# Performance work log

Hardware: AMD Instinct MI355X
Metric: run time of the kernel (lower is better)

The kernel has to match this reference:

```python
import jax, jax.numpy as jnp
import numpy as np

EPS = 1e-9

def setup_inputs() -> dict:
    key = jax.random.key(0)
    k1, k2, k3, k4 = jax.random.split(key, 4)
    B, D, M, R, C = 1024, 16, 4, 4096, 64
    x = jax.random.normal(k1, (B, D), dtype=jnp.float32)
    centers = jax.random.normal(k2, (D, M), dtype=jnp.float32)
    widths = jnp.ones((D, M), dtype=jnp.float32)
    consequents = jax.random.normal(k3, (R, D + 1, C), dtype=jnp.float32)
    rules = jax.random.randint(k4, (R, D), 0, M)  # rule -> MF index per input dim
    return {"x": x, "centers": centers, "widths": widths,
            "consequents": consequents, "rules": rules}

def reference(x, centers, widths, consequents, rules):
    B, D = x.shape
    # Gaussian membership values: [B, D, M]
    mfs = jnp.exp(-(x[:, :, None] - centers[None]) ** 2 / (2.0 * widths[None] ** 2)) + EPS
    # Gather per-rule MFs: rule_mfs[b, d, r] = mfs[b, d, rules[r, d]] -> [B, D, R]
    rule_mfs = jnp.take_along_axis(mfs, rules.T[None, :, :], axis=2)
    # Product firing strengths and normalization: [B, R]
    fs = jnp.prod(rule_mfs, axis=1)
    nfs = fs / (fs.sum(axis=1, keepdims=True) + EPS)
    # Extended input with bias: [B, D+1]
    x_ext = jnp.concatenate([x, jnp.ones((B, 1), dtype=x.dtype)], axis=1)
    # NOTE: faithful to the original torch code: 'bi,rjc->brc' has no shared
    # contraction index, so it sums x_ext over i and consequents over j.
    rule_out = jnp.einsum('br,brc->bc', nfs,
                          jnp.einsum('bi,rjc->brc', x_ext, consequents))
    return rule_out, nfs, x_ext
```

## Files before the change

### kernel.cpp

```cpp
#include <hip/hip_runtime.h>
#include <hip/hip_bf16.h>

typedef __attribute__((ext_vector_type(8))) short short8;
typedef __attribute__((ext_vector_type(4))) short short4v;
typedef __attribute__((ext_vector_type(4))) float floatx4;
typedef __attribute__((ext_vector_type(4))) unsigned int uintx4;
typedef __attribute__((ext_vector_type(4))) int intx4;
typedef unsigned int u32;
typedef unsigned short u16;

#define NB 1024
#define ND 16
#define NM 4
#define NR 4096
#define NC 64
#define EPSF 1e-9f
#define KS 8

__device__ inline u16 f2bf(float f) {
    u32 u;
    __builtin_memcpy(&u, &f, 4);
    u32 lsb = (u >> 16) & 1;
    u += 0x7fffu + lsb;
    return (u16)(u >> 16);
}

__global__ __launch_bounds__(256) void k_pack(const int* __restrict__ rules,
                                              u32* __restrict__ packed) {
    int r = blockIdx.x * 256 + threadIdx.x;
    const int* q = rules + (size_t)r * ND;
    u32 pk = 0;
#pragma unroll
    for (int i = 0; i < 4; ++i) {
        intx4 v = *(const intx4*)(q + i * 4);
#pragma unroll
        for (int e = 0; e < 4; ++e) pk |= ((u32)(v[e] & 3)) << (2 * (i * 4 + e));
    }
    packed[r] = pk;
}

__global__ __launch_bounds__(256) void k_mid(const float* __restrict__ cons,
                                             const float* __restrict__ x,
                                             const float* __restrict__ centers,
                                             const float* __restrict__ widths,
                                             const u32* __restrict__ packed,
                                             u16* __restrict__ s_consT,
                                             float* __restrict__ out_nfs,
                                             float* __restrict__ out_xe,
                                             float* __restrict__ sx) {
    __shared__ u16 tile[16][68];
    __shared__ float xv[16];
    __shared__ float mftab[64];
    __shared__ float gtab[1024];
    __shared__ float wred[4];
    __shared__ float s_inv;
    int bid = blockIdx.x;
    int tid = threadIdx.x;
    if (bid < 256) {
        int rbase = bid * 16;
        int c = tid & 63;
        int rr = tid >> 6;
#pragma unroll
        for (int it = 0; it < 4; ++it, rr += 4) {
            const float* p = cons + (size_t)(rbase + rr) * (ND + 1) * NC + c;
            float s = 0.f;
#pragma unroll
            for (int j = 0; j < ND + 1; ++j) s += p[j * NC];
            tile[rr][c] = f2bf(s);
        }
        __syncthreads();
        int cc = tid >> 2;
        int r0 = (tid & 3) * 4;
        short4v v;
#pragma unroll
        for (int e = 0; e < 4; ++e) v[e] = (short)tile[r0 + e][cc];
        *(short4v*)(s_consT + (size_t)cc * NR + rbase + r0) = v;
        return;
    }
    int b = bid - 256;
    if (tid < 16) {
        float raw = x[b * 16 + tid];
        xv[tid] = raw;
        out_xe[b * 17 + tid] = raw;
    }
    if (tid == 16) out_xe[b * 17 + 16] = 1.0f;
    __syncthreads();
    if (tid < 64) {
        float diff = xv[tid >> 2] - centers[tid];
        float w = widths[tid];
        mftab[tid] = __expf(-diff * diff / (2.f * w * w)) + EPSF;
    }
    __syncthreads();
    for (int idx = tid; idx < 1024; idx += 256) {
        int g = idx >> 8, i = idx & 255;
        const float* mf = mftab + g * 16;
        gtab[idx] = mf[0 + (i & 3)] * mf[4 + ((i >> 2) & 3)] *
                    mf[8 + ((i >> 4) & 3)] * mf[12 + ((i >> 6) & 3)];
    }
    __syncthreads();
    floatx4 f[4];
    float lsum = 0.f;
#pragma unroll
    for (int it = 0; it < 4; ++it) {
        int r = it * 1024 + tid * 4;
        uintx4 p = *(const uintx4*)(packed + r);
#pragma unroll
        for (int e = 0; e < 4; ++e) {
            u32 pk = p[e];
            f[it][e] = gtab[pk & 255] * gtab[256 + ((pk >> 8) & 255)] *
                       gtab[512 + ((pk >> 16) & 255)] * gtab[768 + (pk >> 24)];
            lsum += f[it][e];
        }
    }
    for (int off = 32; off; off >>= 1) lsum += __shfl_down(lsum, off, 64);
    if ((tid & 63) == 0) wred[tid >> 6] = lsum;
    __syncthreads();
    if (tid == 0) s_inv = 1.f / (wred[0] + wred[1] + wred[2] + wred[3] + EPSF);
    __syncthreads();
    float inv = s_inv;
    if (tid == 0) {
        float s = 1.f;
        for (int i = 0; i < 16; ++i) s += xv[i];
        sx[b] = s;
    }
    float* on = out_nfs + (size_t)b * NR;
#pragma unroll
    for (int it = 0; it < 4; ++it) {
        int r = it * 1024 + tid * 4;
        floatx4 v;
#pragma unroll
        for (int e = 0; e < 4; ++e) v[e] = f[it][e] * inv;
        *(floatx4*)(on + r) = v;
    }
}

__global__ __launch_bounds__(256) void k_gemm(const float* __restrict__ nfs,
                                              const u16* __restrict__ s_consT,
                                              float* __restrict__ part) {
    __shared__ float red[2][16][64];
    int rt = blockIdx.x;
    int ks = blockIdx.y;
    int tid = threadIdx.x;
    int wid = tid >> 6, lane = tid & 63;
    int rsub = wid & 1, khalf = wid >> 1;
    int row = rt * 32 + rsub * 16 + (lane & 15);
    int k0 = ks * 512 + khalf * 256 + (lane >> 4) * 8;
    const float* aptr = nfs + (size_t)row * NR + k0;
    const u16* bptr = s_consT + (size_t)(lane & 15) * NR + k0;

    floatx4 acc[4] = {};
    floatx4 a0 = *(const floatx4*)(aptr);
    floatx4 a1 = *(const floatx4*)(aptr + 4);
    short8 bv[4], bn[4];
#pragma unroll
    for (int cb = 0; cb < 4; ++cb) bv[cb] = *(const short8*)(bptr + (size_t)cb * 16 * NR);
#pragma unroll
    for (int t = 0; t < 8; ++t) {
        floatx4 na0, na1;
        if (t < 7) {
            na0 = *(const floatx4*)(aptr + (t + 1) * 32);
            na1 = *(const floatx4*)(aptr + (t + 1) * 32 + 4);
#pragma unroll
            for (int cb = 0; cb < 4; ++cb)
                bn[cb] = *(const short8*)(bptr + (size_t)cb * 16 * NR + (t + 1) * 32);
        }
        short8 af;
#pragma unroll
        for (int e = 0; e < 4; ++e) {
            af[e] = (short)f2bf(a0[e]);
            af[e + 4] = (short)f2bf(a1[e]);
        }
#pragma unroll
        for (int cb = 0; cb < 4; ++cb)
            acc[cb] = __builtin_amdgcn_mfma_f32_16x16x32_bf16(af, bv[cb], acc[cb], 0, 0, 0);
        if (t < 7) {
            a0 = na0; a1 = na1;
#pragma unroll
            for (int cb = 0; cb < 4; ++cb) bv[cb] = bn[cb];
        }
    }
    int rloc = (lane >> 4) * 4;
    if (khalf == 1) {
#pragma unroll
        for (int cb = 0; cb < 4; ++cb)
#pragma unroll
            for (int reg = 0; reg < 4; ++reg)
                red[rsub][rloc + reg][cb * 16 + (lane & 15)] = acc[cb][reg];
    }
    __syncthreads();
    if (khalf == 0) {
        float* po = part + (size_t)ks * (NB * NC);
#pragma unroll
        for (int cb = 0; cb < 4; ++cb)
#pragma unroll
            for (int reg = 0; reg < 4; ++reg) {
                float v = acc[cb][reg] + red[rsub][rloc + reg][cb * 16 + (lane & 15)];
                po[(size_t)(rt * 32 + rsub * 16 + rloc + reg) * NC + cb * 16 + (lane & 15)] = v;
            }
    }
}

__global__ __launch_bounds__(256) void k_out(const float* __restrict__ part,
                                             const float* __restrict__ sx,
                                             float* __restrict__ out0) {
    int t = blockIdx.x * 256 + threadIdx.x;
    float a = 0.f;
#pragma unroll
    for (int ks = 0; ks < KS; ++ks) a += part[(size_t)ks * (NB * NC) + t];
    out0[t] = a * sx[t >> 6];
}

extern "C" void kernel_launch(void* const* d_in, const int* in_sizes, int n_in,
                              void* d_out, int out_size, void* d_ws, size_t ws_size,
                              hipStream_t stream) {
    const float* x = (const float*)d_in[0];
    const float* centers = (const float*)d_in[1];
    const float* widths = (const float*)d_in[2];
    const float* cons = (const float*)d_in[3];
    const int* rules = (const int*)d_in[4];

    float* out = (float*)d_out;
    float* out_rule = out;
    float* out_nfs = out + NB * NC;
    float* out_xe = out + NB * NC + NB * NR;

    char* ws = (char*)d_ws;
    u16* s_consT = (u16*)ws;
    u32* packed = (u32*)(ws + (512 << 10));
    float* sx = (float*)(ws + (512 << 10) + (16 << 10));
    float* part = (float*)(ws + (512 << 10) + (24 << 10));

    k_pack<<<NR / 256, 256, 0, stream>>>(rules, packed);
    k_mid<<<256 + NB, 256, 0, stream>>>(cons, x, centers, widths, packed,
                                        s_consT, out_nfs, out_xe, sx);
    k_gemm<<<dim3(32, KS), 256, 0, stream>>>(out_nfs, s_consT, part);
    k_out<<<(NB * NC) / 256, 256, 0, stream>>>(part, sx, out_rule);
}
```

Before: 31.94 us.

## Widen blocks to 512 threads and double GEMM split-K to 16 slices

```diff
diff --git a/kernel.cpp b/kernel.cpp
--- a/kernel.cpp
+++ b/kernel.cpp
@@ -15,7 +15,7 @@
 #define NR 4096
 #define NC 64
 #define EPSF 1e-9f
-#define KS 8
+#define KS 16
 
 __device__ inline u16 f2bf(float f) {
     u32 u;
@@ -39,7 +39,7 @@
     packed[r] = pk;
 }
 
-__global__ __launch_bounds__(256) void k_mid(const float* __restrict__ cons,
+__global__ __launch_bounds__(512) void k_mid(const float* __restrict__ cons,
                                              const float* __restrict__ x,
                                              const float* __restrict__ centers,
                                              const float* __restrict__ widths,
@@ -48,20 +48,20 @@
                                              float* __restrict__ out_nfs,
                                              float* __restrict__ out_xe,
                                              float* __restrict__ sx) {
-    __shared__ u16 tile[16][68];
+    __shared__ u16 tile[32][68];
     __shared__ float xv[16];
     __shared__ float mftab[64];
     __shared__ float gtab[1024];
-    __shared__ float wred[4];
+    __shared__ float wred[8];
     __shared__ float s_inv;
     int bid = blockIdx.x;
     int tid = threadIdx.x;
-    if (bid < 256) {
-        int rbase = bid * 16;
+    if (bid < 128) {
+        int rbase = bid * 32;
         int c = tid & 63;
         int rr = tid >> 6;
 #pragma unroll
-        for (int it = 0; it < 4; ++it, rr += 4) {
+        for (int it = 0; it < 4; ++it, rr += 8) {
             const float* p = cons + (size_t)(rbase + rr) * (ND + 1) * NC + c;
             float s = 0.f;
 #pragma unroll
@@ -69,15 +69,15 @@
             tile[rr][c] = f2bf(s);
         }
         __syncthreads();
-        int cc = tid >> 2;
-        int r0 = (tid & 3) * 4;
+        int cc = tid >> 3;
+        int r0 = (tid & 7) * 4;
         short4v v;
 #pragma unroll
         for (int e = 0; e < 4; ++e) v[e] = (short)tile[r0 + e][cc];
         *(short4v*)(s_consT + (size_t)cc * NR + rbase + r0) = v;
         return;
     }
-    int b = bid - 256;
+    int b = bid - 128;
     if (tid < 16) {
         float raw = x[b * 16 + tid];
         xv[tid] = raw;
@@ -91,19 +91,21 @@
         mftab[tid] = __expf(-diff * diff / (2.f * w * w)) + EPSF;
     }
     __syncthreads();
-    for (int idx = tid; idx < 1024; idx += 256) {
+#pragma unroll
+    for (int it = 0; it < 2; ++it) {
+        int idx = it * 512 + tid;
         int g = idx >> 8, i = idx & 255;
         const float* mf = mftab + g * 16;
         gtab[idx] = mf[0 + (i & 3)] * mf[4 + ((i >> 2) & 3)] *
                     mf[8 + ((i >> 4) & 3)] * mf[12 + ((i >> 6) & 3)];
     }
     __syncthreads();
-    floatx4 f[4];
+    int r0 = tid * 8;
+    floatx4 f[2];
     float lsum = 0.f;
 #pragma unroll
-    for (int it = 0; it < 4; ++it) {
-        int r = it * 1024 + tid * 4;
-        uintx4 p = *(const uintx4*)(packed + r);
+    for (int it = 0; it < 2; ++it) {
+        uintx4 p = *(const uintx4*)(packed + r0 + it * 4);
 #pragma unroll
         for (int e = 0; e < 4; ++e) {
             u32 pk = p[e];
@@ -115,87 +117,87 @@
     for (int off = 32; off; off >>= 1) lsum += __shfl_down(lsum, off, 64);
     if ((tid & 63) == 0) wred[tid >> 6] = lsum;
     __syncthreads();
-    if (tid == 0) s_inv = 1.f / (wred[0] + wred[1] + wred[2] + wred[3] + EPSF);
+    if (tid == 0) {
+        float t = 0.f;
+#pragma unroll
+        for (int i = 0; i < 8; ++i) t += wred[i];
+        s_inv = 1.f / (t + EPSF);
+    }
     __syncthreads();
     float inv = s_inv;
     if (tid == 0) {
         float s = 1.f;
+#pragma unroll
         for (int i = 0; i < 16; ++i) s += xv[i];
         sx[b] = s;
     }
-    float* on = out_nfs + (size_t)b * NR;
-#pragma unroll
-    for (int it = 0; it < 4; ++it) {
-        int r = it * 1024 + tid * 4;
+    float* on = out_nfs + (size_t)b * NR + r0;
+#pragma unroll
+    for (int it = 0; it < 2; ++it) {
         floatx4 v;
 #pragma unroll
         for (int e = 0; e < 4; ++e) v[e] = f[it][e] * inv;
-        *(floatx4*)(on + r) = v;
-    }
-}
-
-__global__ __launch_bounds__(256) void k_gemm(const float* __restrict__ nfs,
+        *(floatx4*)(on + it * 4) = v;
+    }
+}
+
+__global__ __launch_bounds__(512) void k_gemm(const float* __restrict__ nfs,
                                               const u16* __restrict__ s_consT,
                                               float* __restrict__ part) {
-    __shared__ float red[2][16][64];
+    __shared__ float red[3][2][16][64];
     int rt = blockIdx.x;
     int ks = blockIdx.y;
     int tid = threadIdx.x;
     int wid = tid >> 6, lane = tid & 63;
-    int rsub = wid & 1, khalf = wid >> 1;
+    int rsub = wid & 1, kq = wid >> 1;
     int row = rt * 32 + rsub * 16 + (lane & 15);
-    int k0 = ks * 512 + khalf * 256 + (lane >> 4) * 8;
+    int k0 = ks * 256 + kq * 64 + (lane >> 4) * 8;
     const float* aptr = nfs + (size_t)row * NR + k0;
     const u16* bptr = s_consT + (size_t)(lane & 15) * NR + k0;
 
+    floatx4 a00 = *(const floatx4*)(aptr);
+    floatx4 a01 = *(const floatx4*)(aptr + 4);
+    floatx4 a10 = *(const floatx4*)(aptr + 32);
+    floatx4 a11 = *(const floatx4*)(aptr + 36);
+    short8 b0[4], b1[4];
+#pragma unroll
+    for (int cb = 0; cb < 4; ++cb) {
+        b0[cb] = *(const short8*)(bptr + (size_t)cb * 16 * NR);
+        b1[cb] = *(const short8*)(bptr + (size_t)cb * 16 * NR + 32);
+    }
+    short8 af0, af1;
+#pragma unroll
+    for (int e = 0; e < 4; ++e) {
+        af0[e] = (short)f2bf(a00[e]);
+        af0[e + 4] = (short)f2bf(a01[e]);
+        af1[e] = (short)f2bf(a10[e]);
+        af1[e + 4] = (short)f2bf(a11[e]);
+    }
     floatx4 acc[4] = {};
-    floatx4 a0 = *(const floatx4*)(aptr);
-    floatx4 a1 = *(const floatx4*)(aptr + 4);
-    short8 bv[4], bn[4];
-#pragma unroll
-    for (int cb = 0; cb < 4; ++cb) bv[cb] = *(const short8*)(bptr + (size_t)cb * 16 * NR);
-#pragma unroll
-    for (int t = 0; t < 8; ++t) {
-        floatx4 na0, na1;
-        if (t < 7) {
-            na0 = *(const floatx4*)(aptr + (t + 1) * 32);
-            na1 = *(const floatx4*)(aptr + (t + 1) * 32 + 4);
-#pragma unroll
-            for (int cb = 0; cb < 4; ++cb)
-                bn[cb] = *(const short8*)(bptr + (size_t)cb * 16 * NR + (t + 1) * 32);
-        }
-        short8 af;
-#pragma unroll
-        for (int e = 0; e < 4; ++e) {
-            af[e] = (short)f2bf(a0[e]);
-            af[e + 4] = (short)f2bf(a1[e]);
-        }
+#pragma unroll
+    for (int cb = 0; cb < 4; ++cb) {
+        acc[cb] = __builtin_amdgcn_mfma_f32_16x16x32_bf16(af0, b0[cb], acc[cb], 0, 0, 0);
+        acc[cb] = __builtin_amdgcn_mfma_f32_16x16x32_bf16(af1, b1[cb], acc[cb], 0, 0, 0);
+    }
+    int rloc = (lane >> 4) * 4;
+    if (kq > 0) {
 #pragma unroll
         for (int cb = 0; cb < 4; ++cb)
-            acc[cb] = __builtin_amdgcn_mfma_f32_16x16x32_bf16(af, bv[cb], acc[cb], 0, 0, 0);
-        if (t < 7) {
-            a0 = na0; a1 = na1;
-#pragma unroll
-            for (int cb = 0; cb < 4; ++cb) bv[cb] = bn[cb];
-        }
-    }
-    int rloc = (lane >> 4) * 4;
-    if (khalf == 1) {
+#pragma unroll
+            for (int reg = 0; reg < 4; ++reg)
+                red[kq - 1][rsub][rloc + reg][cb * 16 + (lane & 15)] = acc[cb][reg];
+    }
+    __syncthreads();
+    if (kq == 0) {
+        float* po = part + (size_t)ks * (NB * NC);
 #pragma unroll
         for (int cb = 0; cb < 4; ++cb)
 #pragma unroll
-            for (int reg = 0; reg < 4; ++reg)
-                red[rsub][rloc + reg][cb * 16 + (lane & 15)] = acc[cb][reg];
-    }
-    __syncthreads();
-    if (khalf == 0) {
-        float* po = part + (size_t)ks * (NB * NC);
-#pragma unroll
-        for (int cb = 0; cb < 4; ++cb)
-#pragma unroll
             for (int reg = 0; reg < 4; ++reg) {
-                float v = acc[cb][reg] + red[rsub][rloc + reg][cb * 16 + (lane & 15)];
-                po[(size_t)(rt * 32 + rsub * 16 + rloc + reg) * NC + cb * 16 + (lane & 15)] = v;
+                int rr = rloc + reg, cc = cb * 16 + (lane & 15);
+                float v = acc[cb][reg] + red[0][rsub][rr][cc] +
+                          red[1][rsub][rr][cc] + red[2][rsub][rr][cc];
+                po[(size_t)(rt * 32 + rsub * 16 + rr) * NC + cc] = v;
             }
     }
 }
@@ -231,8 +233,8 @@
     float* part = (float*)(ws + (512 << 10) + (24 << 10));
 
     k_pack<<<NR / 256, 256, 0, stream>>>(rules, packed);
-    k_mid<<<256 + NB, 256, 0, stream>>>(cons, x, centers, widths, packed,
+    k_mid<<<128 + NB, 512, 0, stream>>>(cons, x, centers, widths, packed,
                                         s_consT, out_nfs, out_xe, sx);
-    k_gemm<<<dim3(32, KS), 256, 0, stream>>>(out_nfs, s_consT, part);
+    k_gemm<<<dim3(32, KS), 512, 0, stream>>>(out_nfs, s_consT, part);
     k_out<<<(NB * NC) / 256, 256, 0, stream>>>(part, sx, out_rule);
 }
```

Result: slower. 33.96 us (+6.3%).
